# Kernel tuning notes

Measured on AMD Instinct MI355X. Metric: run time of the kernel, lower is better.

The kernel has to match this reference:

```python
import jax, jax.numpy as jnp
import numpy as np

B, H, S, D = 4, 16, 2048, 128


def setup_inputs() -> dict:
    key = jax.random.key(0)
    kq, kk, kv, km = jax.random.split(key, 4)
    query = jax.random.normal(kq, (B, H, S, D), dtype=jnp.float32)
    k = jax.random.normal(kk, (B, H, S, D), dtype=jnp.float32)
    value = jax.random.normal(kv, (B, H, S, D), dtype=jnp.float32)
    mask = jax.random.randint(km, (B, 1, S, S), 0, 2, dtype=jnp.int32)
    return {"query": query, "key": k, "value": value, "mask": mask, "softmax_dim": -1}


def reference(query, key, value, mask, softmax_dim):
    dk = query.shape[-1]
    # scores: [B, H, S, S]
    scores = jnp.einsum("bhqd,bhkd->bhqk", query, key) / jnp.sqrt(jnp.float32(dk))
    scores = jnp.where(mask == 0, jnp.float32(-1e9), scores)
    attention = jax.nn.softmax(scores, axis=softmax_dim)
    out = jnp.einsum("bhqk,bhkd->bhqd", attention, value)
    return (out, attention)
```

## Files before the change

kernel.cpp:

```cpp
#include <hip/hip_runtime.h>

typedef __attribute__((ext_vector_type(8))) short short8;
typedef __attribute__((ext_vector_type(4))) short short4v;
typedef __attribute__((ext_vector_type(4))) float float4v;

#define B_ 4
#define H_ 16
#define S_ 2048
#define D_ 128
#define BM 64
#define NKT64 32
#define NKT32 64

#define NSH (B_ * H_ * S_ * D_)
#define NMW ((size_t)B_ * 32 * S_)
#define WS_NEED (2ull * (unsigned long long)NSH * 2ull + (unsigned long long)NMW * 8ull)

#define QSCALE (0.08838834764831845f * 1.4426950408889634f)

__device__ __forceinline__ unsigned cvtpk(float lo, float hi) {
  unsigned r;
  asm("v_cvt_pk_bf16_f32 %0, %1, %2" : "=v"(r) : "v"(lo), "v"(hi));
  return r;
}

__device__ __forceinline__ short f2bf(float f) {
  unsigned u = __float_as_uint(f);
  u = (u + 0x7fffu + ((u >> 16) & 1u)) >> 16;
  return (short)u;
}

__device__ __forceinline__ void gl16(const void* g, void* lds) {
  __builtin_amdgcn_global_load_lds(
      (const __attribute__((address_space(1))) unsigned int*)g,
      (__attribute__((address_space(3))) unsigned int*)lds, 16, 0, 0);
}

__global__ void prep_k(const float* __restrict__ Kg, short* __restrict__ Kf) {
  size_t id = (size_t)blockIdx.x * 256 + threadIdx.x;
  int c  = (int)(id & 15);
  int g  = (int)((id >> 4) & 3);
  int dc = (int)((id >> 6) & 3);
  int kf = (int)((id >> 8) & 3);
  int kt = (int)((id >> 10) & 31);
  size_t bh = id >> 15;
  const float* src = Kg + ((bh * S_ + (size_t)(kt * 64 + kf * 16 + c)) * D_) + dc * 32 + g * 8;
  float4v a = *(const float4v*)src;
  float4v b = *(const float4v*)(src + 4);
  int4 s;
  s.x = (int)cvtpk(a[0], a[1]);
  s.y = (int)cvtpk(a[2], a[3]);
  s.z = (int)cvtpk(b[0], b[1]);
  s.w = (int)cvtpk(b[2], b[3]);
  ((int4*)Kf)[id] = s;
}

__global__ void prep_v(const float* __restrict__ Vg, short* __restrict__ Vf) {
  size_t id = (size_t)blockIdx.x * 256 + threadIdx.x;
  int c   = (int)(id & 15);
  int g   = (int)((id >> 4) & 3);
  int df  = (int)((id >> 6) & 7);
  int kt32= (int)((id >> 9) & 63);
  size_t bh = id >> 15;
  const float* src = Vg + (bh * S_ + (size_t)(kt32 * 32 + g * 8)) * D_ + df * 16 + c;
  float f[8];
#pragma unroll
  for (int e = 0; e < 8; ++e) f[e] = src[(size_t)e * D_];
  int4 s;
  s.x = (int)cvtpk(f[0], f[1]);
  s.y = (int)cvtpk(f[2], f[3]);
  s.z = (int)cvtpk(f[4], f[5]);
  s.w = (int)cvtpk(f[6], f[7]);
  ((int4*)Vf)[id] = s;
}

__global__ void prep_m(const int* __restrict__ Mg, unsigned long long* __restrict__ Bits) {
  int gw = blockIdx.x * 4 + (threadIdx.x >> 6);
  int j  = threadIdx.x & 63;
  int kt = gw & 31;
  int q  = (gw >> 5) & (S_ - 1);
  int b  = gw >> 16;
  int m = Mg[((size_t)b * S_ + q) * S_ + kt * 64 + j];
  unsigned long long bal = __ballot(m != 0);
  if (j == 0) Bits[((size_t)b * 32 + kt) * S_ + q] = bal;
}

__global__ __launch_bounds__(256, 4) void sdpa_main(
    const float* __restrict__ Qg, const short* __restrict__ Kfr,
    const short* __restrict__ Vfr, const unsigned long long* __restrict__ Bits,
    float* __restrict__ Og, float* __restrict__ Ag) {

  __shared__ __align__(16) char smem[32768 + 5120];
  short (*Ps)[40] = (short (*)[40])(smem + 32768);

  const int t = threadIdx.x;
  const int w = t >> 6;
  const int l = t & 63;
  const int g = l >> 4;

  const int p    = blockIdx.x;
  const int xcd  = p & 7;
  const int slot = p >> 3;
  const int grp  = ((slot >> 5) << 3) + xcd;
  const int qt   = slot & 31;
  const int h    = grp & 15;
  const int b    = grp >> 4;

  const int qbase  = qt * BM;
  const int qrow_l = w * 16 + (l & 15);
  const int qrow   = qbase + qrow_l;

  const size_t bhOff = (size_t)(b * H_ + h) * (S_ * D_);
  const short* Kp = Kfr + bhOff;
  const short* Vp = Vfr + bhOff;
  const unsigned long long* Bp = Bits + (size_t)b * 32 * S_;
  const unsigned* Bu = (const unsigned*)Bits;
  float* Op = Og + bhOff;
  float* Ap = Ag + (size_t)(b * H_ + h) * ((size_t)S_ * S_);

  short8 qf[4];
#pragma unroll
  for (int dc = 0; dc < 4; ++dc) {
    const float* qsrc = Qg + bhOff + (size_t)qrow * D_ + dc * 32 + g * 8;
    float4v a = *(const float4v*)qsrc;
    float4v c4 = *(const float4v*)(qsrc + 4);
    int4 s;
    s.x = (int)cvtpk(a[0] * QSCALE, a[1] * QSCALE);
    s.y = (int)cvtpk(a[2] * QSCALE, a[3] * QSCALE);
    s.z = (int)cvtpk(c4[0] * QSCALE, c4[1] * QSCALE);
    s.w = (int)cvtpk(c4[2] * QSCALE, c4[3] * QSCALE);
    qf[dc] = *(short8*)&s;
  }

#pragma unroll
  for (int i = 0; i < 4; ++i) {
    int f = w * 4 + i;
    gl16(Kp + f * 512 + l * 8, smem + f * 1024);
  }
  __syncthreads();

  float ls0 = 0.f, ls1 = 0.f, ls2 = 0.f, ls3 = 0.f;
  int cur = 0;
  for (int kt = 0; kt < NKT64; ++kt) {
    if (kt < NKT64 - 1) {
      const short* src = Kp + (size_t)(kt + 1) * 8192;
      char* dst = smem + (cur ^ 1) * 16384;
#pragma unroll
      for (int i = 0; i < 4; ++i) {
        int f = w * 4 + i;
        gl16(src + f * 512 + l * 8, dst + f * 1024);
      }
    }
    unsigned long long mb = Bp[(size_t)kt * S_ + qrow];
    const char* kb = smem + cur * 16384;

    float4v acc[4];
#pragma unroll
    for (int kf = 0; kf < 4; ++kf) acc[kf] = (float4v){0.f, 0.f, 0.f, 0.f};
#pragma unroll
    for (int kf = 0; kf < 4; ++kf) {
#pragma unroll
      for (int dc = 0; dc < 4; ++dc) {
        short8 af = *(const short8*)(kb + (kf * 4 + dc) * 1024 + l * 16);
        acc[kf] = __builtin_amdgcn_mfma_f32_16x16x32_bf16(af, qf[dc], acc[kf], 0, 0, 0);
      }
    }
#pragma unroll
    for (int kf = 0; kf < 4; ++kf) {
      unsigned mg = (unsigned)(mb >> (kf * 16 + g * 4)) & 0xFu;
      float p0 = ((mg >> 0) & 1) ? __builtin_amdgcn_exp2f(acc[kf][0]) : 0.f;
      float p1 = ((mg >> 1) & 1) ? __builtin_amdgcn_exp2f(acc[kf][1]) : 0.f;
      float p2 = ((mg >> 2) & 1) ? __builtin_amdgcn_exp2f(acc[kf][2]) : 0.f;
      float p3 = ((mg >> 3) & 1) ? __builtin_amdgcn_exp2f(acc[kf][3]) : 0.f;
      if (kf == 0) ls0 += (p0 + p1) + (p2 + p3);
      else if (kf == 1) ls1 += (p0 + p1) + (p2 + p3);
      else if (kf == 2) ls2 += (p0 + p1) + (p2 + p3);
      else ls3 += (p0 + p1) + (p2 + p3);
    }
    __syncthreads();
    cur ^= 1;
  }
  float lsum = (ls0 + ls1) + (ls2 + ls3);
  lsum += __shfl_xor(lsum, 16);
  lsum += __shfl_xor(lsum, 32);
  const float lg = (lsum > 0.f) ? __log2f(lsum) : 1e30f;

#pragma unroll
  for (int i = 0; i < 2; ++i) {
    int f = w + 4 * i;
    gl16(Kp + f * 512 + l * 8, smem + f * 1024);
    gl16(Vp + f * 512 + l * 8, smem + 16384 + f * 1024);
  }
  __syncthreads();

  float4v acco[8];
#pragma unroll
  for (int df = 0; df < 8; ++df) acco[df] = (float4v){0.f, 0.f, 0.f, 0.f};

  cur = 0;
  for (int kt = 0; kt < NKT32; ++kt) {
    if (kt < NKT32 - 1) {
      const short* ks = Kp + (size_t)(kt + 1) * 4096;
      const short* vs = Vp + (size_t)(kt + 1) * 4096;
      char* kd = smem + (cur ^ 1) * 8192;
      char* vd = smem + 16384 + (cur ^ 1) * 8192;
#pragma unroll
      for (int i = 0; i < 2; ++i) {
        int f = w + 4 * i;
        gl16(ks + f * 512 + l * 8, kd + f * 1024);
        gl16(vs + f * 512 + l * 8, vd + f * 1024);
      }
    }
    unsigned mw = Bu[((size_t)(b * 32 + (kt >> 1)) * S_ + qrow) * 2 + (kt & 1)];
    const char* kb = smem + cur * 8192;
    const char* vb = smem + 16384 + cur * 8192;

    float4v acc[2];
#pragma unroll
    for (int kf = 0; kf < 2; ++kf) acc[kf] = (float4v){0.f, 0.f, 0.f, 0.f};
#pragma unroll
    for (int kf = 0; kf < 2; ++kf) {
#pragma unroll
      for (int dc = 0; dc < 4; ++dc) {
        short8 af = *(const short8*)(kb + (kf * 4 + dc) * 1024 + l * 16);
        acc[kf] = __builtin_amdgcn_mfma_f32_16x16x32_bf16(af, qf[dc], acc[kf], 0, 0, 0);
      }
    }

#pragma unroll
    for (int kf = 0; kf < 2; ++kf) {
      int k0 = kt * 32 + kf * 16 + g * 4;
      unsigned mg = (mw >> (kf * 16 + g * 4)) & 0xFu;
      float4v aw;
#pragma unroll
      for (int r = 0; r < 4; ++r) {
        float arg = ((mg >> r) & 1) ? (acc[kf][r] - lg) : -1e30f;
        aw[r] = __builtin_amdgcn_exp2f(arg);
      }
      int2 pb;
      pb.x = (int)cvtpk(aw[0], aw[1]);
      pb.y = (int)cvtpk(aw[2], aw[3]);
      __builtin_nontemporal_store(aw, (float4v*)(Ap + (size_t)qrow * S_ + k0));
      *(int2*)&Ps[qrow_l][kf * 16 + g * 4] = pb;
    }

    {
      short8 pbf = *(const short8*)&Ps[qrow_l][g * 8];
#pragma unroll
      for (int df = 0; df < 8; ++df) {
        short8 vf = *(const short8*)(vb + df * 1024 + l * 16);
        acco[df] = __builtin_amdgcn_mfma_f32_16x16x32_bf16(vf, pbf, acco[df], 0, 0, 0);
      }
    }
    __syncthreads();
    cur ^= 1;
  }

#pragma unroll
  for (int df = 0; df < 8; ++df) {
    __builtin_nontemporal_store(acco[df], (float4v*)(Op + (size_t)qrow * D_ + df * 16 + g * 4));
  }
}

#define LQK 136
#define LVT 72

__global__ __launch_bounds__(256, 3) void sdpa_fallback(
    const float* __restrict__ Qg, const float* __restrict__ Kg,
    const float* __restrict__ Vg, const int* __restrict__ Mg,
    float* __restrict__ Og, float* __restrict__ Ag) {

  __shared__ __align__(16) char smemf[17408 + 27648];
  short (*Ks)[LQK]  = (short (*)[LQK])(smemf);
  short (*Qs)[LQK]  = (short (*)[LQK])(smemf + 17408);
  short (*VTs)[LVT] = (short (*)[LVT])(smemf + 17408);
  short (*Psf)[LVT] = (short (*)[LVT])(smemf + 17408 + 18432);

  const int t = threadIdx.x;
  const int w = t >> 6;
  const int l = t & 63;
  const int g = l >> 4;
  const int c = l & 15;

  const int bid = blockIdx.x;
  const int qt = bid & 31;
  const int h  = (bid >> 5) & 15;
  const int b  = bid >> 9;

  const int qbase  = qt * BM;
  const int qrow_l = w * 16 + c;
  const int qrow   = qbase + qrow_l;

  const size_t bhOff = (size_t)(b * H_ + h) * (S_ * D_);
  const float* Qp = Qg + bhOff;
  const float* Kp = Kg + bhOff;
  const float* Vp = Vg + bhOff;
  const int*   Mp = Mg + (size_t)b * S_ * S_;
  float* Op = Og + bhOff;
  float* Ap = Ag + (size_t)(b * H_ + h) * ((size_t)S_ * S_);

#pragma unroll
  for (int i = 0; i < 8; ++i) {
    int idx = t + i * 256;
    int d4 = idx & 31, row = idx >> 5;
    float4v v = *(const float4v*)(Qp + (size_t)(qbase + row) * D_ + d4 * 4);
    short4v s;
    s[0] = f2bf(v[0] * QSCALE); s[1] = f2bf(v[1] * QSCALE);
    s[2] = f2bf(v[2] * QSCALE); s[3] = f2bf(v[3] * QSCALE);
    *(short4v*)&Qs[row][d4 * 4] = s;
  }
  __syncthreads();

  short8 qf[4];
#pragma unroll
  for (int dc = 0; dc < 4; ++dc)
    qf[dc] = *(const short8*)&Qs[qrow_l][dc * 32 + g * 8];

  float m_run = -1e30f, l_run = 0.f;
  for (int kt = 0; kt < 32; ++kt) {
    __syncthreads();
#pragma unroll
    for (int i = 0; i < 8; ++i) {
      int idx = t + i * 256;
      int d4 = idx & 31, row = idx >> 5;
      float4v v = *(const float4v*)(Kp + (size_t)(kt * 64 + row) * D_ + d4 * 4);
      short4v s;
      s[0] = f2bf(v[0]); s[1] = f2bf(v[1]); s[2] = f2bf(v[2]); s[3] = f2bf(v[3]);
      *(short4v*)&Ks[row][d4 * 4] = s;
    }
    __syncthreads();

    float4v acc[4];
#pragma unroll
    for (int kf = 0; kf < 4; ++kf) acc[kf] = (float4v){0.f, 0.f, 0.f, 0.f};
#pragma unroll
    for (int kf = 0; kf < 4; ++kf) {
#pragma unroll
      for (int dc = 0; dc < 4; ++dc) {
        short8 af = *(const short8*)&Ks[kf * 16 + c][dc * 32 + g * 8];
        acc[kf] = __builtin_amdgcn_mfma_f32_16x16x32_bf16(af, qf[dc], acc[kf], 0, 0, 0);
      }
    }

    float sv[4][4];
    float tmax = -1e30f;
#pragma unroll
    for (int kf = 0; kf < 4; ++kf) {
      int k0 = kt * 64 + kf * 16 + g * 4;
      const int4 mv = *(const int4*)(Mp + (size_t)qrow * S_ + k0);
      int mr[4] = {mv.x, mv.y, mv.z, mv.w};
#pragma unroll
      for (int r = 0; r < 4; ++r) {
        float x = acc[kf][r];
        x = (mr[r] == 0) ? -1e9f : x;
        sv[kf][r] = x;
        tmax = fmaxf(tmax, x);
      }
    }
    tmax = fmaxf(tmax, __shfl_xor(tmax, 16));
    tmax = fmaxf(tmax, __shfl_xor(tmax, 32));
    float newm = fmaxf(m_run, tmax);
    float tsum = 0.f;
#pragma unroll
    for (int kf = 0; kf < 4; ++kf)
#pragma unroll
      for (int r = 0; r < 4; ++r)
        tsum += __builtin_amdgcn_exp2f(sv[kf][r] - newm);
    tsum += __shfl_xor(tsum, 16);
    tsum += __shfl_xor(tsum, 32);
    l_run = l_run * __builtin_amdgcn_exp2f(m_run - newm) + tsum;
    m_run = newm;
  }

  const float rl = 1.0f / l_run;

  float4v acco[8];
#pragma unroll
  for (int df = 0; df < 8; ++df) acco[df] = (float4v){0.f, 0.f, 0.f, 0.f};

  for (int kt = 0; kt < 32; ++kt) {
    __syncthreads();
#pragma unroll
    for (int i = 0; i < 8; ++i) {
      int idx = t + i * 256;
      int d4 = idx & 31, row = idx >> 5;
      float4v v = *(const float4v*)(Kp + (size_t)(kt * 64 + row) * D_ + d4 * 4);
      short4v s;
      s[0] = f2bf(v[0]); s[1] = f2bf(v[1]); s[2] = f2bf(v[2]); s[3] = f2bf(v[3]);
      *(short4v*)&Ks[row][d4 * 4] = s;
    }
#pragma unroll
    for (int i = 0; i < 8; ++i) {
      int idx = t + i * 256;
      int d = idx & 127, kq = idx >> 7;
      const float* vp = Vp + (size_t)(kt * 64 + kq * 4) * D_ + d;
      short4v s;
      s[0] = f2bf(vp[0]); s[1] = f2bf(vp[D_]); s[2] = f2bf(vp[2 * D_]); s[3] = f2bf(vp[3 * D_]);
      *(short4v*)&VTs[d][kq * 4] = s;
    }
    __syncthreads();

    float4v acc[4];
#pragma unroll
    for (int kf = 0; kf < 4; ++kf) acc[kf] = (float4v){0.f, 0.f, 0.f, 0.f};
#pragma unroll
    for (int kf = 0; kf < 4; ++kf) {
#pragma unroll
      for (int dc = 0; dc < 4; ++dc) {
        short8 af = *(const short8*)&Ks[kf * 16 + c][dc * 32 + g * 8];
        acc[kf] = __builtin_amdgcn_mfma_f32_16x16x32_bf16(af, qf[dc], acc[kf], 0, 0, 0);
      }
    }

#pragma unroll
    for (int kf = 0; kf < 4; ++kf) {
      int k0 = kt * 64 + kf * 16 + g * 4;
      const int4 mv = *(const int4*)(Mp + (size_t)qrow * S_ + k0);
      int mr[4] = {mv.x, mv.y, mv.z, mv.w};
      float4v aw;
      short4v pb;
#pragma unroll
      for (int r = 0; r < 4; ++r) {
        float x = acc[kf][r];
        x = (mr[r] == 0) ? -1e9f : x;
        float pn = __builtin_amdgcn_exp2f(x - m_run) * rl;
        aw[r] = pn;
        pb[r] = f2bf(pn);
      }
      __builtin_nontemporal_store(aw, (float4v*)(Ap + (size_t)qrow * S_ + k0));
      *(short4v*)&Psf[qrow_l][kf * 16 + g * 4] = pb;
    }

#pragma unroll
    for (int kc = 0; kc < 2; ++kc) {
      short8 pbf = *(const short8*)&Psf[qrow_l][kc * 32 + g * 8];
#pragma unroll
      for (int df = 0; df < 8; ++df) {
        short8 vf = *(const short8*)&VTs[df * 16 + c][kc * 32 + g * 8];
        acco[df] = __builtin_amdgcn_mfma_f32_16x16x32_bf16(vf, pbf, acco[df], 0, 0, 0);
      }
    }
  }

#pragma unroll
  for (int df = 0; df < 8; ++df) {
    *(float4v*)(Op + (size_t)qrow * D_ + df * 16 + g * 4) = acco[df];
  }
}

extern "C" void kernel_launch(void* const* d_in, const int* in_sizes, int n_in,
                              void* d_out, int out_size, void* d_ws, size_t ws_size,
                              hipStream_t stream) {
  const float* Q = (const float*)d_in[0];
  const float* K = (const float*)d_in[1];
  const float* V = (const float*)d_in[2];
  const int*   M = (const int*)d_in[3];
  float* Out  = (float*)d_out;
  float* Attn = Out + (size_t)B_ * H_ * S_ * D_;

  if (ws_size >= WS_NEED) {
    short* Kf = (short*)d_ws;
    short* Vf = Kf + (size_t)NSH;
    unsigned long long* Bits = (unsigned long long*)(Vf + (size_t)NSH);
    const int pgrid = NSH / 8 / 256;
    prep_k<<<dim3(pgrid), dim3(256), 0, stream>>>(K, Kf);
    prep_v<<<dim3(pgrid), dim3(256), 0, stream>>>(V, Vf);
    prep_m<<<dim3((unsigned)(NMW / 4)), dim3(256), 0, stream>>>(M, Bits);
    sdpa_main<<<dim3(B_ * H_ * (S_ / BM)), dim3(256), 0, stream>>>(
        Q, Kf, Vf, Bits, Out, Attn);
  } else {
    sdpa_fallback<<<dim3(B_ * H_ * (S_ / BM)), dim3(256), 0, stream>>>(Q, K, V, M, Out, Attn);
  }
}
```

Measured before the change: 433.5 us.

## Replace LDS P staging with ds_bpermute shuffles and prefetch mask bits

The bf16 probability fragment is now rearranged for the PV MFMA with in-wave ds_bpermute shuffles instead of being written to and read back from a shared-memory P tile. This removes the extra LDS buffer, which allows the launch bound to rise from 4 to 5 blocks per CU. Mask bit words are also loaded one iteration ahead to hide global-load latency. In exchange there are eight bpermutes per tile, plus higher register pressure from the prefetch under a tighter occupancy bound, which could cause spills.

```diff
diff --git a/kernel.cpp b/kernel.cpp
--- a/kernel.cpp
+++ b/kernel.cpp
@@ -85,13 +85,12 @@
   if (j == 0) Bits[((size_t)b * 32 + kt) * S_ + q] = bal;
 }
 
-__global__ __launch_bounds__(256, 4) void sdpa_main(
+__global__ __launch_bounds__(256, 5) void sdpa_main(
     const float* __restrict__ Qg, const short* __restrict__ Kfr,
     const short* __restrict__ Vfr, const unsigned long long* __restrict__ Bits,
     float* __restrict__ Og, float* __restrict__ Ag) {
 
-  __shared__ __align__(16) char smem[32768 + 5120];
-  short (*Ps)[40] = (short (*)[40])(smem + 32768);
+  __shared__ __align__(16) char smem[32768];
 
   const int t = threadIdx.x;
   const int w = t >> 6;
@@ -117,6 +116,10 @@
   const unsigned* Bu = (const unsigned*)Bits;
   float* Op = Og + bhOff;
   float* Ap = Ag + (size_t)(b * H_ + h) * ((size_t)S_ * S_);
+
+  const int a01 = ((((l >> 4) & 1) * 2) * 16 + (l & 15)) * 4;
+  const int a23 = a01 + 64;
+  const bool hiHalf = (l >= 32);
 
   short8 qf[4];
 #pragma unroll
@@ -140,9 +143,12 @@
   __syncthreads();
 
   float ls0 = 0.f, ls1 = 0.f, ls2 = 0.f, ls3 = 0.f;
+  unsigned long long mb = Bp[qrow];
   int cur = 0;
   for (int kt = 0; kt < NKT64; ++kt) {
+    unsigned long long mb_next = 0;
     if (kt < NKT64 - 1) {
+      mb_next = Bp[(size_t)(kt + 1) * S_ + qrow];
       const short* src = Kp + (size_t)(kt + 1) * 8192;
       char* dst = smem + (cur ^ 1) * 16384;
 #pragma unroll
@@ -151,7 +157,6 @@
         gl16(src + f * 512 + l * 8, dst + f * 1024);
       }
     }
-    unsigned long long mb = Bp[(size_t)kt * S_ + qrow];
     const char* kb = smem + cur * 16384;
 
     float4v acc[4];
@@ -178,6 +183,7 @@
       else ls3 += (p0 + p1) + (p2 + p3);
     }
     __syncthreads();
+    mb = mb_next;
     cur ^= 1;
   }
   float lsum = (ls0 + ls1) + (ls2 + ls3);
@@ -197,9 +203,12 @@
 #pragma unroll
   for (int df = 0; df < 8; ++df) acco[df] = (float4v){0.f, 0.f, 0.f, 0.f};
 
+  unsigned mw = Bu[((size_t)(b * 32) * S_ + qrow) * 2];
   cur = 0;
   for (int kt = 0; kt < NKT32; ++kt) {
+    unsigned mw_next = 0;
     if (kt < NKT32 - 1) {
+      mw_next = Bu[((size_t)(b * 32 + ((kt + 1) >> 1)) * S_ + qrow) * 2 + ((kt + 1) & 1)];
       const short* ks = Kp + (size_t)(kt + 1) * 4096;
       const short* vs = Vp + (size_t)(kt + 1) * 4096;
       char* kd = smem + (cur ^ 1) * 8192;
@@ -211,7 +220,6 @@
         gl16(vs + f * 512 + l * 8, vd + f * 1024);
       }
     }
-    unsigned mw = Bu[((size_t)(b * 32 + (kt >> 1)) * S_ + qrow) * 2 + (kt & 1)];
     const char* kb = smem + cur * 8192;
     const char* vb = smem + 16384 + cur * 8192;
 
@@ -227,6 +235,7 @@
       }
     }
 
+    unsigned wv[2][2];
 #pragma unroll
     for (int kf = 0; kf < 2; ++kf) {
       int k0 = kt * 32 + kf * 16 + g * 4;
@@ -237,22 +246,35 @@
         float arg = ((mg >> r) & 1) ? (acc[kf][r] - lg) : -1e30f;
         aw[r] = __builtin_amdgcn_exp2f(arg);
       }
-      int2 pb;
-      pb.x = (int)cvtpk(aw[0], aw[1]);
-      pb.y = (int)cvtpk(aw[2], aw[3]);
+      wv[kf][0] = cvtpk(aw[0], aw[1]);
+      wv[kf][1] = cvtpk(aw[2], aw[3]);
       __builtin_nontemporal_store(aw, (float4v*)(Ap + (size_t)qrow * S_ + k0));
-      *(int2*)&Ps[qrow_l][kf * 16 + g * 4] = pb;
-    }
-
+    }
+
+    int4 pi;
     {
-      short8 pbf = *(const short8*)&Ps[qrow_l][g * 8];
-#pragma unroll
-      for (int df = 0; df < 8; ++df) {
-        short8 vf = *(const short8*)(vb + df * 1024 + l * 16);
-        acco[df] = __builtin_amdgcn_mfma_f32_16x16x32_bf16(vf, pbf, acco[df], 0, 0, 0);
-      }
-    }
-    __syncthreads();
+      int l00 = __builtin_amdgcn_ds_bpermute(a01, (int)wv[0][0]);
+      int h00 = __builtin_amdgcn_ds_bpermute(a01, (int)wv[1][0]);
+      int l01 = __builtin_amdgcn_ds_bpermute(a01, (int)wv[0][1]);
+      int h01 = __builtin_amdgcn_ds_bpermute(a01, (int)wv[1][1]);
+      int l10 = __builtin_amdgcn_ds_bpermute(a23, (int)wv[0][0]);
+      int h10 = __builtin_amdgcn_ds_bpermute(a23, (int)wv[1][0]);
+      int l11 = __builtin_amdgcn_ds_bpermute(a23, (int)wv[0][1]);
+      int h11 = __builtin_amdgcn_ds_bpermute(a23, (int)wv[1][1]);
+      pi.x = hiHalf ? h00 : l00;
+      pi.y = hiHalf ? h01 : l01;
+      pi.z = hiHalf ? h10 : l10;
+      pi.w = hiHalf ? h11 : l11;
+    }
+    short8 pbf = *(short8*)&pi;
+
+#pragma unroll
+    for (int df = 0; df < 8; ++df) {
+      short8 vf = *(const short8*)(vb + df * 1024 + l * 16);
+      acco[df] = __builtin_amdgcn_mfma_f32_16x16x32_bf16(vf, pbf, acco[df], 0, 0, 0);
+    }
+    __syncthreads();
+    mw = mw_next;
     cur ^= 1;
   }
 
```

After: 454.7 us. 4.9% more time.
